# Kernel optimization log

Measured on AMD Instinct MI355X. Metric: run time of the kernel, lower is better.

## Reference

```python
import jax, jax.numpy as jnp
import numpy as np
from jax import lax

EPS = 1e-4
DN = ('NDHWC', 'DHWIO', 'NDHWC')


def _m(mask, dtype):
    return mask[..., None].astype(dtype)


def bn_relu(x, mask):
    # BatchNorm1d over active voxels only (training-mode batch stats, gamma=1, beta=0), then ReLU.
    m = _m(mask, x.dtype)
    n = jnp.sum(m)
    mean = jnp.sum(x * m, axis=(0, 1, 2, 3)) / n
    xc = (x - mean) * m  # re-mask: inactive voxels stay exactly zero
    var = jnp.sum(xc * xc, axis=(0, 1, 2, 3)) / n
    return jnp.maximum(xc * lax.rsqrt(var + EPS), 0.0)


def subm3(x, w, mask):
    # SubMConv3d k=3 pad=1: dense conv on zero-at-inactive input, output restricted to active sites.
    y = lax.conv_general_dilated(x, w, (1, 1, 1), 'SAME', dimension_numbers=DN)
    return y * _m(mask, x.dtype)


def down2(x, w):
    # SparseConv3d k=2 s=2: non-overlapping windows; inactive inputs are zero so dense strided conv matches.
    return lax.conv_general_dilated(x, w, (2, 2, 2), 'VALID', dimension_numbers=DN)


def pool_mask(mask):
    B, D, H, W = mask.shape
    return jnp.any(mask.reshape(B, D // 2, 2, H // 2, 2, W // 2, 2), axis=(2, 4, 6))


def up2(x, w, mask):
    # SparseInverseConv3d k=2 (indice_key inverse of the stride-2 conv): conv-transpose masked to original indices.
    y = jnp.einsum('bdhwc,ijkco->bdihjwko', x, w)
    B, Dc, _, Hc, _, Wc, _, Co = y.shape
    return y.reshape(B, 2 * Dc, 2 * Hc, 2 * Wc, Co) * _m(mask, x.dtype)


def resblock(x, mask, wa, wb, w_sc=None):
    # ResidualBlock: i_branch (identity or 1x1 Custom1x1Subm3d: feats @ W.T) + BN-ReLU-SubM-BN-ReLU-SubM.
    idb = x if w_sc is None else jnp.einsum('bdhwc,oc->bdhwo', x, w_sc)
    h = bn_relu(x, mask)
    h = subm3(h, wa, mask)
    h = bn_relu(h, mask)
    h = subm3(h, wb, mask)
    return h + idb


def unet_forward(x, mask, w_in, w_b1a, w_b1b, w_d1, w_b2a, w_b2b, w_d2,
                 w_b3a, w_b3b, w_u2, w_t2_sc, w_t2a, w_t2b, w_u1, w_t1_sc, w_t1a, w_t1b):
    mask2 = pool_mask(mask)
    mask3 = pool_mask(mask2)
    x0 = subm3(x, w_in, mask)                 # input_conv (subm1)
    x1 = resblock(x0, mask, w_b1a, w_b1b)     # level-1 block (32->32)
    d1 = down2(bn_relu(x1, mask), w_d1)       # BN-ReLU + stride-2 conv 32->64
    x2 = resblock(d1, mask2, w_b2a, w_b2b)    # level-2 block (64->64)
    d2 = down2(bn_relu(x2, mask2), w_d2)      # 64->96
    x3 = resblock(d2, mask3, w_b3a, w_b3b)    # bottom level (96->96)
    u2 = up2(bn_relu(x3, mask3), w_u2, mask2)  # BN-ReLU + inverse conv 96->64
    t2 = resblock(jnp.concatenate([x2, u2], -1), mask2, w_t2a, w_t2b, w_t2_sc)  # tail 128->64
    u1 = up2(bn_relu(t2, mask2), w_u1, mask)   # 64->32
    t1 = resblock(jnp.concatenate([x1, u1], -1), mask, w_t1a, w_t1b, w_t1_sc)   # tail 64->32
    return bn_relu(t1, mask)                   # output_layer: BN + ReLU


def setup_inputs() -> dict:
    key = jax.random.key(0)
    ks = jax.random.split(key, 20)
    B, D = 1, 48
    Cin, C1, C2, C3 = 6, 32, 64, 96
    mask = jax.random.uniform(ks[0], (B, D, D, D)) < 0.12
    x = jax.random.normal(ks[1], (B, D, D, D, Cin), jnp.float32) * mask[..., None]

    def w(k, shape):
        fan = float(np.prod(shape[:-1]))
        return (jax.random.normal(k, shape, jnp.float32) / np.sqrt(fan)).astype(jnp.float32)

    return {
        'x': x, 'mask': mask,
        'w_in': w(ks[2], (3, 3, 3, Cin, C1)),
        'w_b1a': w(ks[3], (3, 3, 3, C1, C1)), 'w_b1b': w(ks[4], (3, 3, 3, C1, C1)),
        'w_d1': w(ks[5], (2, 2, 2, C1, C2)),
        'w_b2a': w(ks[6], (3, 3, 3, C2, C2)), 'w_b2b': w(ks[7], (3, 3, 3, C2, C2)),
        'w_d2': w(ks[8], (2, 2, 2, C2, C3)),
        'w_b3a': w(ks[9], (3, 3, 3, C3, C3)), 'w_b3b': w(ks[10], (3, 3, 3, C3, C3)),
        'w_u2': w(ks[11], (2, 2, 2, C3, C2)),
        'w_t2_sc': w(ks[12], (C2, 2 * C2)),
        'w_t2a': w(ks[13], (3, 3, 3, 2 * C2, C2)), 'w_t2b': w(ks[14], (3, 3, 3, C2, C2)),
        'w_u1': w(ks[15], (2, 2, 2, C2, C1)),
        'w_t1_sc': w(ks[16], (C1, 2 * C1)),
        'w_t1a': w(ks[17], (3, 3, 3, 2 * C1, C1)), 'w_t1b': w(ks[18], (3, 3, 3, C1, C1)),
    }


def reference(x, mask, w_in, w_b1a, w_b1b, w_d1, w_b2a, w_b2b, w_d2,
              w_b3a, w_b3b, w_u2, w_t2_sc, w_t2a, w_t2b, w_u1, w_t1_sc, w_t1a, w_t1b):
    return unet_forward(x, mask, w_in, w_b1a, w_b1b, w_d1, w_b2a, w_b2b, w_d2,
                        w_b3a, w_b3b, w_u2, w_t2_sc, w_t2a, w_t2b, w_u1, w_t1_sc, w_t1a, w_t1b)
```

## Files before the change

### kernel.cpp

```cpp
#include <hip/hip_runtime.h>


typedef short bf16x8 __attribute__((ext_vector_type(8)));
typedef float f32x4 __attribute__((ext_vector_type(4)));
typedef unsigned short ushort_t;

constexpr int D1 = 48, DIM2 = 24, DIM3 = 12;
constexpr int N1 = D1 * D1 * D1;
constexpr int N2 = DIM2 * DIM2 * DIM2;
constexpr int N3 = DIM3 * DIM3 * DIM3;

constexpr size_t OFF_A      = 0;
constexpr size_t OFF_R1     = 3538944;
constexpr size_t OFF_CAT1   = 7077888;
constexpr size_t OFF_D1R    = 14155776;
constexpr size_t OFF_R3     = 15040512;
constexpr size_t OFF_CAT2   = 15925248;
constexpr size_t OFF_D2R    = 17694720;
constexpr size_t OFF_R4     = 17860608;
constexpr size_t OFF_X3R    = 18026496;
constexpr size_t OFF_BN1_32 = 18192384;
constexpr size_t OFF_BN1_64 = 19961920;
constexpr size_t OFF_BN2_A  = 23500928;
constexpr size_t OFF_BN2_B  = 23943360;
constexpr size_t OFF_BN3_96 = 24385792;
constexpr size_t OFF_BFEND  = 24468800;
constexpr size_t OFF_WT     = 24468800;
constexpr size_t OFF_STATS  = 25142592;
constexpr size_t STATS_FLOATS = 16 * 4096;
constexpr size_t OFF_CNT    = OFF_STATS + STATS_FLOATS;
constexpr size_t OFF_L1     = OFF_CNT + 16;
constexpr size_t OFF_L2     = OFF_L1 + N1;
constexpr size_t OFF_L3     = OFF_L2 + N2;
constexpr size_t OFF_M1     = OFF_L3 + N3;
constexpr size_t OFF_M2     = OFF_M1 + N1 / 4;
constexpr size_t OFF_M3     = OFF_M2 + N2 / 4;

constexpr int WTS[17] = {0, 27648, 55296, 82944, 99328, 209920, 320512,
                         369664, 618496, 867328, 977920, 1088512, 1199104,
                         1254400, 1282048, 1331200, 1347584};

__device__ inline ushort_t f2bf(float f) {
  union { float f; unsigned u; } x; x.f = f;
  unsigned u = x.u + 0x7FFF + ((x.u >> 16) & 1);
  return (ushort_t)(u >> 16);
}

__global__ __launch_bounds__(256) void k_mask1(const float* __restrict__ x,
                                               unsigned char* __restrict__ m,
                                               int* __restrict__ list, int* __restrict__ cnt) {
  int v = blockIdx.x * 256 + threadIdx.x;
  if (v >= N1) return;
  const float* p = x + (size_t)v * 6;
  bool a = (p[0] != 0.f) || (p[1] != 0.f) || (p[2] != 0.f) ||
           (p[3] != 0.f) || (p[4] != 0.f) || (p[5] != 0.f);
  m[v] = a ? 1 : 0;
  if (a) { int pos = atomicAdd(cnt, 1); list[pos] = v; }
}

__global__ __launch_bounds__(256) void k_pool(const unsigned char* __restrict__ mf,
                                              unsigned char* __restrict__ mc,
                                              int* __restrict__ list, int* __restrict__ cnt, int DC) {
  int v = blockIdx.x * 256 + threadIdx.x;
  int n = DC * DC * DC;
  if (v >= n) return;
  int w = v % DC, h = (v / DC) % DC, d = v / (DC * DC);
  int DF = 2 * DC;
  bool a = false;
  for (int i = 0; i < 2; i++)
    for (int j = 0; j < 2; j++)
      for (int k = 0; k < 2; k++)
        a |= (mf[(size_t)(((2 * d + i) * DF + (2 * h + j)) * DF + (2 * w + k))] != 0);
  mc[v] = a ? 1 : 0;
  if (a) { int pos = atomicAdd(cnt, 1); list[pos] = v; }
}

struct WJobs {
  const float* src[16];
  int start[17];
  short cirtot[16], cio[16], cipad[16], cout[16];
};

__global__ __launch_bounds__(256) void k_wprep(WJobs jb, ushort_t* __restrict__ wt, int total) {
  int gid = blockIdx.x * 256 + threadIdx.x;
  if (gid >= total) return;
  int j = 0;
#pragma unroll
  for (int jj = 0; jj < 16; jj++)
    if (gid >= jb.start[jj + 1]) j = jj + 1;
  int e = gid - jb.start[j];
  int CIP = jb.cipad[j], CO = jb.cout[j];
  int CIRT = jb.cirtot[j], CIO = jb.cio[j];
  int ci = e % CIP;
  int co = (e / CIP) % CO;
  int k = e / (CIP * CO);
  float v = (ci + CIO < CIRT) ? jb.src[j][((size_t)k * CIRT + CIO + ci) * CO + co] : 0.f;
  wt[gid] = f2bf(v);
}

__global__ __launch_bounds__(256) void k_xprep(const float* __restrict__ x, ushort_t* __restrict__ xp) {
  int gid = blockIdx.x * 256 + threadIdx.x;
  if (gid >= (N1 + 4) * 8) return;
  int v = gid >> 3, c = (gid & 7) * 4;
  uint2 o = make_uint2(0u, 0u);
  if (v < N1) {
    ushort_t u[4];
#pragma unroll
    for (int j = 0; j < 4; j++) {
      int ci = c + j;
      float f = (ci < 6) ? x[(size_t)v * 6 + ci] : 0.f;
      u[j] = f2bf(f);
    }
    o.x = (unsigned)u[0] | ((unsigned)u[1] << 16);
    o.y = (unsigned)u[2] | ((unsigned)u[3] << 16);
  }
  *(uint2*)&xp[(size_t)v * 32 + c] = o;
}

template <int CIPAD, int CB, int KK, int DD, bool UP>
__global__ __launch_bounds__(512, 2) void k_conv7(
    const ushort_t* __restrict__ in, const ushort_t* __restrict__ wt, int cot,
    float* __restrict__ out, int ostride, int ooff,
    const float* __restrict__ res, int rstride,
    double* __restrict__ st,
    const int* __restrict__ list, const int* __restrict__ cnt) {
  constexpr int KCH = CIPAD / 32;
  constexpr int NCO = CB / 16;
  constexpr int TPS = (KK + 3) / 4;
  constexpr int BUNITS = KK * KCH * CB * 4;
  __shared__ ushort_t blds[BUNITS * 8];
  __shared__ float red[4][2][NCO * 4][64];
  __shared__ float sred0[CB], sred1[CB];
  __shared__ int vidx[32];

  int n = cnt[0];
  int t = threadIdx.x, wv = t >> 6, ln = t & 63;
  int vg = wv & 1, ks = wv >> 1;
  int fr = ln & 15, kg = ln >> 4;
  int coblk = blockIdx.y * CB;

  for (int e = t; e < BUNITS; e += 512) {
    int kgs = e & 3;
    int co = (e >> 2) % CB;
    int r2 = (e >> 2) / CB;
    int c = r2 % KCH;
    int k = r2 / KCH;
    bf16x8 w = *(const bf16x8*)(wt + ((size_t)k * cot + coblk + co) * CIPAD + c * 32 + kgs * 8);
    *(bf16x8*)(blds + (size_t)e * 8) = w;
  }
  if (t < CB) { sred0[t] = 0.f; sred1[t] = 0.f; }
  __syncthreads();

  float smr = 0.f, sqr = 0.f;
  int myco = ((t >> 8) % NCO) * 16 + (t & 15);

  for (int tile = blockIdx.x; tile * 32 < n; tile += gridDim.x) {
    int base = tile * 32;
    if (t < 32) vidx[t] = (base + t < n) ? list[base + t] : -1;
    __syncthreads();

    int av = vidx[vg * 16 + fr];
    int vv = av < 0 ? 0 : av;
    int ad = vv / (DD * DD), ah = (vv / DD) % DD, aw = vv % DD;
    int pidx = 0, corner = -1;
    if (UP) {
      constexpr int DC = DD / 2;
      pidx = (((ad >> 1) * DC) + (ah >> 1)) * DC + (aw >> 1);
      corner = ((ad & 1) << 2) | ((ah & 1) << 1) | (aw & 1);
    }
    constexpr int GDI = UP ? (DD / 2) : ((KK == 8) ? 2 * DD : DD);
    constexpr int SENT = GDI * GDI * GDI;

    const int k0 = ks * TPS;
    auto nixOf = [&](int kq) -> int {
      int kc = (kq < KK) ? kq : KK - 1;
      if (UP) {
        return (av >= 0 && corner == kc) ? pidx : SENT;
      } else if (KK == 27) {
        int kd = kc / 9 - 1, kh = (kc / 3) % 3 - 1, kw = kc % 3 - 1;
        int nd = ad + kd, nh = ah + kh, nw = aw + kw;
        bool inb = (av >= 0) && (unsigned)nd < (unsigned)DD &&
                   (unsigned)nh < (unsigned)DD && (unsigned)nw < (unsigned)DD;
        return inb ? (nd * DD + nh) * DD + nw : SENT;
      } else {
        return (av >= 0) ? ((2 * ad + ((kc >> 2) & 1)) * GDI + (2 * ah + ((kc >> 1) & 1))) * GDI +
                               (2 * aw + (kc & 1))
                         : SENT;
      }
    };
    auto loadA = [&](bf16x8* dst, int kq) {
      int nix = nixOf(kq);
      const ushort_t* ap = in + (size_t)nix * CIPAD + kg * 8;
#pragma unroll
      for (int c = 0; c < KCH; c++) dst[c] = *(const bf16x8*)(ap + c * 32);
    };

    f32x4 acc[NCO];
#pragma unroll
    for (int f = 0; f < NCO; f++) acc[f] = (f32x4){0.f, 0.f, 0.f, 0.f};

    bf16x8 aA[KCH], aB[KCH];
    loadA(aA, k0);
#pragma unroll
    for (int j = 0; j < TPS; j++) {
      bf16x8* cur = (j & 1) ? aB : aA;
      bf16x8* nxt = (j & 1) ? aA : aB;
      if (j + 1 < TPS) loadA(nxt, k0 + j + 1);
      if (k0 + j < KK) {
#pragma unroll
        for (int c = 0; c < KCH; c++) {
#pragma unroll
          for (int f = 0; f < NCO; f++) {
            bf16x8 b = *(const bf16x8*)(blds +
                ((((size_t)((k0 + j) * KCH + c) * CB) + f * 16 + fr) * 4 + kg) * 8);
            acc[f] = __builtin_amdgcn_mfma_f32_16x16x32_bf16(cur[c], b, acc[f], 0, 0, 0);
          }
        }
      }
    }

#pragma unroll
    for (int f = 0; f < NCO; f++)
#pragma unroll
      for (int r = 0; r < 4; r++)
        red[ks][vg][f * 4 + r][ln] = acc[f][r];
    __syncthreads();

#pragma unroll
    for (int e0 = 0; e0 < NCO; e0++) {
      int e = t + e0 * 512;
      int ln2 = e & 63, r = (e >> 6) & 3;
      int f = (e >> 8) % NCO;
      int vg2 = e / (256 * NCO);
      int ei = f * 4 + r;
      float s = red[0][vg2][ei][ln2] + red[1][vg2][ei][ln2] +
                red[2][vg2][ei][ln2] + red[3][vg2][ei][ln2];
      int slot = vg2 * 16 + (ln2 >> 4) * 4 + r;
      int co = f * 16 + (ln2 & 15);
      int v = vidx[slot];
      if (v >= 0) {
        int gco = coblk + co;
        float val = s;
        if (res) val += res[(size_t)v * rstride + gco];
        out[(size_t)v * ostride + ooff + gco] = val;
        smr += val; sqr += val * val;
      }
    }
    __syncthreads();
  }

  atomicAdd(&sred0[myco], smr);
  atomicAdd(&sred1[myco], sqr);
  __syncthreads();
  if (t < CB) {
    double* sr = st + (size_t)(blockIdx.x & 7) * 256;
    atomicAdd(&sr[coblk + t], (double)sred0[t]);
    atomicAdd(&sr[128 + coblk + t], (double)sred1[t]);
  }
}

template <int C>
__global__ __launch_bounds__(256) void k_bnapply2(
    const float* __restrict__ x, int xstr, int coff,
    const double* __restrict__ sA, const double* __restrict__ sB, int csplit,
    const int* __restrict__ list, const int* __restrict__ cnt,
    ushort_t* __restrict__ out) {
  __shared__ float mu_s[C], inv_s[C];
  int n = cnt[0];
  int t = threadIdx.x;
  if (t < C) {
    const double* s = (t < csplit) ? (sA + t) : (sB + (t - csplit));
    double sm = 0.0, sq = 0.0;
#pragma unroll
    for (int r = 0; r < 8; r++) { sm += s[r * 256]; sq += s[r * 256 + 128]; }
    double mu = sm / n;
    double var = sq / n - mu * mu;
    mu_s[t] = (float)mu;
    inv_s[t] = rsqrtf((float)fmax(var, 0.0) + 1e-4f);
  }
  __syncthreads();
  int total = n * (C / 4);
  for (int gid = blockIdx.x * 256 + t; gid < total; gid += gridDim.x * 256) {
    int i = gid / (C / 4);
    int c = (gid % (C / 4)) * 4;
    int v = list[i];
    float4 xv = *(const float4*)&x[(size_t)v * xstr + coff + c];
    float xa[4] = {xv.x, xv.y, xv.z, xv.w};
    ushort_t u[4];
#pragma unroll
    for (int j = 0; j < 4; j++)
      u[j] = f2bf(fmaxf((xa[j] - mu_s[c + j]) * inv_s[c + j], 0.f));
    uint2 o; o.x = (unsigned)u[0] | ((unsigned)u[1] << 16);
    o.y = (unsigned)u[2] | ((unsigned)u[3] << 16);
    *(uint2*)&out[(size_t)v * C + c] = o;
  }
}

__global__ __launch_bounds__(256) void k_bnout(const float* __restrict__ x,
                                               const unsigned char* __restrict__ m,
                                               const double* __restrict__ s,
                                               const int* __restrict__ cnt,
                                               float* __restrict__ out) {
  __shared__ float mu_s[32], inv_s[32];
  int t = threadIdx.x;
  int n = cnt[0];
  if (t < 32) {
    double sm = 0.0, sq = 0.0;
#pragma unroll
    for (int r = 0; r < 8; r++) { sm += s[r * 256 + t]; sq += s[r * 256 + 128 + t]; }
    double mu = sm / n;
    double var = sq / n - mu * mu;
    mu_s[t] = (float)mu;
    inv_s[t] = rsqrtf((float)fmax(var, 0.0) + 1e-4f);
  }
  __syncthreads();
  int gid = blockIdx.x * 256 + t;
  if (gid >= N1 * 8) return;
  int v = gid / 8;
  int c = (gid % 8) * 4;
  float4 o = make_float4(0.f, 0.f, 0.f, 0.f);
  if (m[v]) {
    float4 xv = *(const float4*)&x[(size_t)v * 32 + c];
    o.x = fmaxf((xv.x - mu_s[c + 0]) * inv_s[c + 0], 0.f);
    o.y = fmaxf((xv.y - mu_s[c + 1]) * inv_s[c + 1], 0.f);
    o.z = fmaxf((xv.z - mu_s[c + 2]) * inv_s[c + 2], 0.f);
    o.w = fmaxf((xv.w - mu_s[c + 3]) * inv_s[c + 3], 0.f);
  }
  *(float4*)&out[(size_t)v * 32 + c] = o;
}

template <int CI, int CO>
__global__ __launch_bounds__(256) void k_sc(const float* __restrict__ in,
                                            const float* __restrict__ wsc,
                                            float* __restrict__ out,
                                            const int* __restrict__ list,
                                            const int* __restrict__ cnt) {
  int n = cnt[0];
  long total = (long)n * CO;
  for (long gid = (long)blockIdx.x * 256 + threadIdx.x; gid < total; gid += (long)gridDim.x * 256) {
    int i = (int)(gid / CO), o = (int)(gid % CO);
    int v = list[i];
    const float4* xr = (const float4*)(in + (size_t)v * CI);
    const float4* wr = (const float4*)(wsc + (size_t)o * CI);
    float a = 0.f;
    for (int c = 0; c < CI / 4; c++) {
      float4 x4 = xr[c], w4 = wr[c];
      a += x4.x * w4.x + x4.y * w4.y + x4.z * w4.z + x4.w * w4.w;
    }
    out[(size_t)v * CO + o] = a;
  }
}

extern "C" void kernel_launch(void* const* d_in, const int* in_sizes, int n_in,
                              void* d_out, int out_size, void* d_ws, size_t ws_size,
                              hipStream_t stream) {
  float* W = (float*)d_ws;
  const float* x = (const float*)d_in[0];

  float* A    = W + OFF_A;
  float* R1   = W + OFF_R1;
  float* CAT1 = W + OFF_CAT1;
  float* D1R  = W + OFF_D1R;
  float* R3   = W + OFF_R3;
  float* CAT2 = W + OFF_CAT2;
  float* D2R  = W + OFF_D2R;
  float* R4   = W + OFF_R4;
  float* X3R  = W + OFF_X3R;
  ushort_t* XP     = (ushort_t*)(W + OFF_CAT1);
  ushort_t* BN1_32 = (ushort_t*)(W + OFF_BN1_32);
  ushort_t* BN1_64 = (ushort_t*)(W + OFF_BN1_64);
  ushort_t* BN2A   = (ushort_t*)(W + OFF_BN2_A);
  ushort_t* BN2B   = (ushort_t*)(W + OFF_BN2_B);
  ushort_t* BN3_96 = (ushort_t*)(W + OFF_BN3_96);
  ushort_t* WT  = (ushort_t*)(W + OFF_WT);
  double* S0 = (double*)(W + OFF_STATS);
  int* CNT = (int*)(W + OFF_CNT);
  int* L1 = (int*)(W + OFF_L1);
  int* L2 = (int*)(W + OFF_L2);
  int* L3 = (int*)(W + OFF_L3);
  unsigned char* M1 = (unsigned char*)(W + OFF_M1);
  unsigned char* M2 = (unsigned char*)(W + OFF_M2);
  unsigned char* M3 = (unsigned char*)(W + OFF_M3);

  auto S = [&](int i) { return S0 + (size_t)i * 2048; };

  hipMemsetAsync(W + OFF_STATS, 0, (STATS_FLOATS + 16) * 4, stream);
  hipMemsetAsync(W + OFF_BN1_32, 0, (OFF_BFEND - OFF_BN1_32) * 4, stream);

  k_mask1<<<N1 / 256, 256, 0, stream>>>(x, M1, L1, CNT + 0);
  k_pool<<<N2 / 256, 256, 0, stream>>>(M1, M2, L2, CNT + 1, DIM2);
  k_pool<<<(N3 + 255) / 256, 256, 0, stream>>>(M2, M3, L3, CNT + 2, DIM3);

  WJobs jb;
  const int srcIdx[16]  = {2, 3, 4, 5, 6, 7, 8, 9, 10, 13, 13, 14, 17, 18, 11, 15};
  const short cirtot[16]= {6, 32, 32, 32, 64, 64, 64, 96, 96, 128, 128, 64, 64, 32, 96, 64};
  const short cio[16]   = {0, 0, 0, 0, 0, 0, 0, 0, 0, 0, 64, 0, 0, 0, 0, 0};
  const short cipad[16] = {32, 32, 32, 32, 64, 64, 64, 96, 96, 64, 64, 64, 64, 32, 96, 64};
  const short couts[16] = {32, 32, 32, 64, 64, 64, 96, 96, 96, 64, 64, 64, 32, 32, 64, 32};
  for (int j = 0; j < 16; j++) {
    jb.src[j] = (const float*)d_in[srcIdx[j]];
    jb.cirtot[j] = cirtot[j]; jb.cio[j] = cio[j];
    jb.cipad[j] = cipad[j]; jb.cout[j] = couts[j];
    jb.start[j] = WTS[j];
  }
  jb.start[16] = WTS[16];
  k_wprep<<<(WTS[16] + 255) / 256, 256, 0, stream>>>(jb, WT, WTS[16]);
  k_xprep<<<((N1 + 4) * 8 + 255) / 256, 256, 0, stream>>>(x, XP);

  const int BNG = 512;

  k_conv7<32, 32, 27, D1, false><<<dim3(256, 1), 512, 0, stream>>>(
      XP, WT + WTS[0], 32, A, 32, 0, nullptr, 0, S(0), L1, CNT + 0);
  k_bnapply2<32><<<BNG, 256, 0, stream>>>(A, 32, 0, S(0), S(0), 32, L1, CNT + 0, BN1_32);
  k_conv7<32, 32, 27, D1, false><<<dim3(256, 1), 512, 0, stream>>>(
      BN1_32, WT + WTS[1], 32, R1, 32, 0, nullptr, 0, S(1), L1, CNT + 0);
  k_bnapply2<32><<<BNG, 256, 0, stream>>>(R1, 32, 0, S(1), S(1), 32, L1, CNT + 0, BN1_32);
  k_conv7<32, 32, 27, D1, false><<<dim3(256, 1), 512, 0, stream>>>(
      BN1_32, WT + WTS[2], 32, CAT1, 64, 0, A, 32, S(2), L1, CNT + 0);
  k_bnapply2<32><<<BNG, 256, 0, stream>>>(CAT1, 64, 0, S(2), S(2), 32, L1, CNT + 0, BN1_32);
  k_conv7<32, 32, 8, DIM2, false><<<dim3(128, 2), 512, 0, stream>>>(
      BN1_32, WT + WTS[3], 64, D1R, 64, 0, nullptr, 0, S(3), L2, CNT + 1);

  k_bnapply2<64><<<BNG, 256, 0, stream>>>(D1R, 64, 0, S(3), S(3), 64, L2, CNT + 1, BN2A);
  k_conv7<64, 32, 27, DIM2, false><<<dim3(128, 2), 512, 0, stream>>>(
      BN2A, WT + WTS[4], 64, R3, 64, 0, nullptr, 0, S(4), L2, CNT + 1);
  k_bnapply2<64><<<BNG, 256, 0, stream>>>(R3, 64, 0, S(4), S(4), 64, L2, CNT + 1, BN2A);
  k_conv7<64, 32, 27, DIM2, false><<<dim3(128, 2), 512, 0, stream>>>(
      BN2A, WT + WTS[5], 64, CAT2, 128, 0, D1R, 64, S(5), L2, CNT + 1);
  k_bnapply2<64><<<BNG, 256, 0, stream>>>(CAT2, 128, 0, S(5), S(5), 64, L2, CNT + 1, BN2A);
  k_conv7<64, 32, 8, DIM3, false><<<dim3(54, 3), 512, 0, stream>>>(
      BN2A, WT + WTS[6], 96, D2R, 96, 0, nullptr, 0, S(6), L3, CNT + 2);

  k_bnapply2<96><<<BNG, 256, 0, stream>>>(D2R, 96, 0, S(6), S(6), 96, L3, CNT + 2, BN3_96);
  k_conv7<96, 16, 27, DIM3, false><<<dim3(54, 6), 512, 0, stream>>>(
      BN3_96, WT + WTS[7], 96, R4, 96, 0, nullptr, 0, S(7), L3, CNT + 2);
  k_bnapply2<96><<<BNG, 256, 0, stream>>>(R4, 96, 0, S(7), S(7), 96, L3, CNT + 2, BN3_96);
  k_conv7<96, 16, 27, DIM3, false><<<dim3(54, 6), 512, 0, stream>>>(
      BN3_96, WT + WTS[8], 96, X3R, 96, 0, D2R, 96, S(8), L3, CNT + 2);
  k_bnapply2<96><<<BNG, 256, 0, stream>>>(X3R, 96, 0, S(8), S(8), 96, L3, CNT + 2, BN3_96);
  k_conv7<96, 32, 8, DIM2, true><<<dim3(128, 2), 512, 0, stream>>>(
      BN3_96, WT + WTS[14], 64, CAT2, 128, 64, nullptr, 0, S(9), L2, CNT + 1);

  k_bnapply2<64><<<BNG, 256, 0, stream>>>(CAT2, 128, 64, S(9), S(9), 64, L2, CNT + 1, BN2B);
  k_conv7<64, 32, 27, DIM2, false><<<dim3(128, 2), 512, 0, stream>>>(
      BN2A, WT + WTS[9], 64, R3, 64, 0, nullptr, 0, S(15), L2, CNT + 1);
  k_conv7<64, 32, 27, DIM2, false><<<dim3(128, 2), 512, 0, stream>>>(
      BN2B, WT + WTS[10], 64, R3, 64, 0, R3, 64, S(10), L2, CNT + 1);
  k_bnapply2<64><<<BNG, 256, 0, stream>>>(R3, 64, 0, S(10), S(10), 64, L2, CNT + 1, BN2A);
  k_sc<128, 64><<<512, 256, 0, stream>>>(CAT2, (const float*)d_in[12], D1R, L2, CNT + 1);
  k_conv7<64, 32, 27, DIM2, false><<<dim3(128, 2), 512, 0, stream>>>(
      BN2A, WT + WTS[11], 64, R3, 64, 0, D1R, 64, S(11), L2, CNT + 1);
  k_bnapply2<64><<<BNG, 256, 0, stream>>>(R3, 64, 0, S(11), S(11), 64, L2, CNT + 1, BN2A);
  k_conv7<64, 32, 8, D1, true><<<dim3(256, 1), 512, 0, stream>>>(
      BN2A, WT + WTS[15], 32, CAT1, 64, 32, nullptr, 0, S(12), L1, CNT + 0);

  k_bnapply2<64><<<BNG, 256, 0, stream>>>(CAT1, 64, 0, S(2), S(12), 32, L1, CNT + 0, BN1_64);
  k_conv7<64, 32, 27, D1, false><<<dim3(256, 1), 512, 0, stream>>>(
      BN1_64, WT + WTS[12], 32, R1, 32, 0, nullptr, 0, S(13), L1, CNT + 0);
  k_bnapply2<32><<<BNG, 256, 0, stream>>>(R1, 32, 0, S(13), S(13), 32, L1, CNT + 0, BN1_32);
  k_sc<64, 32><<<512, 256, 0, stream>>>(CAT1, (const float*)d_in[16], A, L1, CNT + 0);
  k_conv7<32, 32, 27, D1, false><<<dim3(256, 1), 512, 0, stream>>>(
      BN1_32, WT + WTS[13], 32, A, 32, 0, A, 32, S(14), L1, CNT + 0);
  k_bnout<<<N1 * 8 / 256, 256, 0, stream>>>(A, M1, S(14), CNT + 0, (float*)d_out);
}
```

Baseline: 391.6 us.

## Hold conv weights in registers instead of LDS and parameterize voxel-group split

The sparse conv kernel now loads each wave's slice of the weights straight into registers (indexed by its tap range) instead of staging all taps in shared memory and reading B fragments from LDS inside the MFMA loop. A new VG template parameter controls how the 8 waves divide between voxel groups and tap splits. Channel-block sizes and grid shapes for several layers are retuned to match. This removes the LDS weight staging, its barrier and the per-MFMA LDS reads, but raises register pressure (up to TPS*KCH*NCO bf16x8 per lane), which could cause spills or lower occupancy under launch_bounds(512,2).

```diff
diff --git a/kernel.cpp b/kernel.cpp
--- a/kernel.cpp
+++ b/kernel.cpp
@@ -117,8 +117,8 @@
   *(uint2*)&xp[(size_t)v * 32 + c] = o;
 }
 
-template <int CIPAD, int CB, int KK, int DD, bool UP>
-__global__ __launch_bounds__(512, 2) void k_conv7(
+template <int CIPAD, int CB, int KK, int VG, int DD, bool UP>
+__global__ __launch_bounds__(512, 2) void k_conv8(
     const ushort_t* __restrict__ in, const ushort_t* __restrict__ wt, int cot,
     float* __restrict__ out, int ostride, int ooff,
     const float* __restrict__ res, int rstride,
@@ -126,37 +126,45 @@
     const int* __restrict__ list, const int* __restrict__ cnt) {
   constexpr int KCH = CIPAD / 32;
   constexpr int NCO = CB / 16;
-  constexpr int TPS = (KK + 3) / 4;
-  constexpr int BUNITS = KK * KCH * CB * 4;
-  __shared__ ushort_t blds[BUNITS * 8];
-  __shared__ float red[4][2][NCO * 4][64];
+  constexpr int KS = 8 / VG;
+  constexpr int TPS = (KK + KS - 1) / KS;
+  constexpr int TILE = VG * 16;
+  constexpr int ETOT = VG * NCO * 256;
+  constexpr int NE = (ETOT + 511) / 512;
+  __shared__ float red[KS][VG][NCO * 4][64];
   __shared__ float sred0[CB], sred1[CB];
-  __shared__ int vidx[32];
+  __shared__ int vidx[TILE];
 
   int n = cnt[0];
   int t = threadIdx.x, wv = t >> 6, ln = t & 63;
-  int vg = wv & 1, ks = wv >> 1;
+  int vg = wv % VG, ks = wv / VG;
   int fr = ln & 15, kg = ln >> 4;
   int coblk = blockIdx.y * CB;
-
-  for (int e = t; e < BUNITS; e += 512) {
-    int kgs = e & 3;
-    int co = (e >> 2) % CB;
-    int r2 = (e >> 2) / CB;
-    int c = r2 % KCH;
-    int k = r2 / KCH;
-    bf16x8 w = *(const bf16x8*)(wt + ((size_t)k * cot + coblk + co) * CIPAD + c * 32 + kgs * 8);
-    *(bf16x8*)(blds + (size_t)e * 8) = w;
+  int k0 = ks * TPS;
+
+  bf16x8 wr[TPS][KCH][NCO];
+#pragma unroll
+  for (int j = 0; j < TPS; j++) {
+    int kk = k0 + j;
+    int kc = (kk < KK) ? kk : KK - 1;
+#pragma unroll
+    for (int c = 0; c < KCH; c++)
+#pragma unroll
+      for (int f = 0; f < NCO; f++)
+        wr[j][c][f] = *(const bf16x8*)(wt +
+            ((size_t)kc * cot + coblk + f * 16 + fr) * CIPAD + c * 32 + kg * 8);
   }
   if (t < CB) { sred0[t] = 0.f; sred1[t] = 0.f; }
-  __syncthreads();
 
   float smr = 0.f, sqr = 0.f;
   int myco = ((t >> 8) % NCO) * 16 + (t & 15);
 
-  for (int tile = blockIdx.x; tile * 32 < n; tile += gridDim.x) {
-    int base = tile * 32;
-    if (t < 32) vidx[t] = (base + t < n) ? list[base + t] : -1;
+  constexpr int GDI = UP ? (DD / 2) : ((KK == 8) ? 2 * DD : DD);
+  constexpr int SENT = GDI * GDI * GDI;
+
+  for (int tile = blockIdx.x; tile * TILE < n; tile += gridDim.x) {
+    int base = tile * TILE;
+    if (t < TILE) vidx[t] = (base + t < n) ? list[base + t] : -1;
     __syncthreads();
 
     int av = vidx[vg * 16 + fr];
@@ -168,28 +176,26 @@
       pidx = (((ad >> 1) * DC) + (ah >> 1)) * DC + (aw >> 1);
       corner = ((ad & 1) << 2) | ((ah & 1) << 1) | (aw & 1);
     }
-    constexpr int GDI = UP ? (DD / 2) : ((KK == 8) ? 2 * DD : DD);
-    constexpr int SENT = GDI * GDI * GDI;
-
-    const int k0 = ks * TPS;
+
     auto nixOf = [&](int kq) -> int {
       int kc = (kq < KK) ? kq : KK - 1;
+      bool tapv = (kq < KK) && (av >= 0);
       if (UP) {
-        return (av >= 0 && corner == kc) ? pidx : SENT;
+        return (tapv && corner == kc) ? pidx : SENT;
       } else if (KK == 27) {
         int kd = kc / 9 - 1, kh = (kc / 3) % 3 - 1, kw = kc % 3 - 1;
         int nd = ad + kd, nh = ah + kh, nw = aw + kw;
-        bool inb = (av >= 0) && (unsigned)nd < (unsigned)DD &&
+        bool inb = tapv && (unsigned)nd < (unsigned)DD &&
                    (unsigned)nh < (unsigned)DD && (unsigned)nw < (unsigned)DD;
         return inb ? (nd * DD + nh) * DD + nw : SENT;
       } else {
-        return (av >= 0) ? ((2 * ad + ((kc >> 2) & 1)) * GDI + (2 * ah + ((kc >> 1) & 1))) * GDI +
-                               (2 * aw + (kc & 1))
-                         : SENT;
+        return tapv ? ((2 * ad + ((kc >> 2) & 1)) * GDI + (2 * ah + ((kc >> 1) & 1))) * GDI +
+                          (2 * aw + (kc & 1))
+                    : SENT;
       }
     };
-    auto loadA = [&](bf16x8* dst, int kq) {
-      int nix = nixOf(kq);
+    auto loadA = [&](bf16x8* dst, int j) {
+      int nix = nixOf(k0 + j);
       const ushort_t* ap = in + (size_t)nix * CIPAD + kg * 8;
 #pragma unroll
       for (int c = 0; c < KCH; c++) dst[c] = *(const bf16x8*)(ap + c * 32);
@@ -200,23 +206,16 @@
     for (int f = 0; f < NCO; f++) acc[f] = (f32x4){0.f, 0.f, 0.f, 0.f};
 
     bf16x8 aA[KCH], aB[KCH];
-    loadA(aA, k0);
+    loadA(aA, 0);
 #pragma unroll
     for (int j = 0; j < TPS; j++) {
+      if (j + 1 < TPS) loadA((j & 1) ? aA : aB, j + 1);
       bf16x8* cur = (j & 1) ? aB : aA;
-      bf16x8* nxt = (j & 1) ? aA : aB;
-      if (j + 1 < TPS) loadA(nxt, k0 + j + 1);
-      if (k0 + j < KK) {
-#pragma unroll
-        for (int c = 0; c < KCH; c++) {
-#pragma unroll
-          for (int f = 0; f < NCO; f++) {
-            bf16x8 b = *(const bf16x8*)(blds +
-                ((((size_t)((k0 + j) * KCH + c) * CB) + f * 16 + fr) * 4 + kg) * 8);
-            acc[f] = __builtin_amdgcn_mfma_f32_16x16x32_bf16(cur[c], b, acc[f], 0, 0, 0);
-          }
-        }
-      }
+#pragma unroll
+      for (int c = 0; c < KCH; c++)
+#pragma unroll
+        for (int f = 0; f < NCO; f++)
+          acc[f] = __builtin_amdgcn_mfma_f32_16x16x32_bf16(cur[c], wr[j][c][f], acc[f], 0, 0, 0);
     }
 
 #pragma unroll
@@ -227,23 +226,25 @@
     __syncthreads();
 
 #pragma unroll
-    for (int e0 = 0; e0 < NCO; e0++) {
+    for (int e0 = 0; e0 < NE; e0++) {
       int e = t + e0 * 512;
-      int ln2 = e & 63, r = (e >> 6) & 3;
-      int f = (e >> 8) % NCO;
-      int vg2 = e / (256 * NCO);
-      int ei = f * 4 + r;
-      float s = red[0][vg2][ei][ln2] + red[1][vg2][ei][ln2] +
-                red[2][vg2][ei][ln2] + red[3][vg2][ei][ln2];
-      int slot = vg2 * 16 + (ln2 >> 4) * 4 + r;
-      int co = f * 16 + (ln2 & 15);
-      int v = vidx[slot];
-      if (v >= 0) {
-        int gco = coblk + co;
-        float val = s;
-        if (res) val += res[(size_t)v * rstride + gco];
-        out[(size_t)v * ostride + ooff + gco] = val;
-        smr += val; sqr += val * val;
+      if (e < ETOT) {
+        int ln2 = e & 63, r = (e >> 6) & 3;
+        int f = (e >> 8) % NCO;
+        int vg2 = e / (256 * NCO);
+        float s = 0.f;
+#pragma unroll
+        for (int q = 0; q < KS; q++) s += red[q][vg2][f * 4 + r][ln2];
+        int slot = vg2 * 16 + (ln2 >> 4) * 4 + r;
+        int co = f * 16 + (ln2 & 15);
+        int v = vidx[slot];
+        if (v >= 0) {
+          int gco = coblk + co;
+          float val = s;
+          if (res) val += res[(size_t)v * rstride + gco];
+          out[(size_t)v * ostride + ooff + gco] = val;
+          smr += val; sqr += val * val;
+        }
       }
     }
     __syncthreads();
@@ -409,57 +410,57 @@
 
   const int BNG = 512;
 
-  k_conv7<32, 32, 27, D1, false><<<dim3(256, 1), 512, 0, stream>>>(
+  k_conv8<32, 32, 27, 2, D1, false><<<dim3(256, 1), 512, 0, stream>>>(
       XP, WT + WTS[0], 32, A, 32, 0, nullptr, 0, S(0), L1, CNT + 0);
   k_bnapply2<32><<<BNG, 256, 0, stream>>>(A, 32, 0, S(0), S(0), 32, L1, CNT + 0, BN1_32);
-  k_conv7<32, 32, 27, D1, false><<<dim3(256, 1), 512, 0, stream>>>(
+  k_conv8<32, 32, 27, 2, D1, false><<<dim3(256, 1), 512, 0, stream>>>(
       BN1_32, WT + WTS[1], 32, R1, 32, 0, nullptr, 0, S(1), L1, CNT + 0);
   k_bnapply2<32><<<BNG, 256, 0, stream>>>(R1, 32, 0, S(1), S(1), 32, L1, CNT + 0, BN1_32);
-  k_conv7<32, 32, 27, D1, false><<<dim3(256, 1), 512, 0, stream>>>(
+  k_conv8<32, 32, 27, 2, D1, false><<<dim3(256, 1), 512, 0, stream>>>(
       BN1_32, WT + WTS[2], 32, CAT1, 64, 0, A, 32, S(2), L1, CNT + 0);
   k_bnapply2<32><<<BNG, 256, 0, stream>>>(CAT1, 64, 0, S(2), S(2), 32, L1, CNT + 0, BN1_32);
-  k_conv7<32, 32, 8, DIM2, false><<<dim3(128, 2), 512, 0, stream>>>(
+  k_conv8<32, 32, 8, 2, DIM2, false><<<dim3(160, 2), 512, 0, stream>>>(
       BN1_32, WT + WTS[3], 64, D1R, 64, 0, nullptr, 0, S(3), L2, CNT + 1);
 
   k_bnapply2<64><<<BNG, 256, 0, stream>>>(D1R, 64, 0, S(3), S(3), 64, L2, CNT + 1, BN2A);
-  k_conv7<64, 32, 27, DIM2, false><<<dim3(128, 2), 512, 0, stream>>>(
+  k_conv8<64, 16, 27, 2, DIM2, false><<<dim3(96, 4), 512, 0, stream>>>(
       BN2A, WT + WTS[4], 64, R3, 64, 0, nullptr, 0, S(4), L2, CNT + 1);
   k_bnapply2<64><<<BNG, 256, 0, stream>>>(R3, 64, 0, S(4), S(4), 64, L2, CNT + 1, BN2A);
-  k_conv7<64, 32, 27, DIM2, false><<<dim3(128, 2), 512, 0, stream>>>(
+  k_conv8<64, 16, 27, 2, DIM2, false><<<dim3(96, 4), 512, 0, stream>>>(
       BN2A, WT + WTS[5], 64, CAT2, 128, 0, D1R, 64, S(5), L2, CNT + 1);
   k_bnapply2<64><<<BNG, 256, 0, stream>>>(CAT2, 128, 0, S(5), S(5), 64, L2, CNT + 1, BN2A);
-  k_conv7<64, 32, 8, DIM3, false><<<dim3(54, 3), 512, 0, stream>>>(
+  k_conv8<64, 32, 8, 2, DIM3, false><<<dim3(54, 3), 512, 0, stream>>>(
       BN2A, WT + WTS[6], 96, D2R, 96, 0, nullptr, 0, S(6), L3, CNT + 2);
 
   k_bnapply2<96><<<BNG, 256, 0, stream>>>(D2R, 96, 0, S(6), S(6), 96, L3, CNT + 2, BN3_96);
-  k_conv7<96, 16, 27, DIM3, false><<<dim3(54, 6), 512, 0, stream>>>(
+  k_conv8<96, 16, 27, 1, DIM3, false><<<dim3(108, 6), 512, 0, stream>>>(
       BN3_96, WT + WTS[7], 96, R4, 96, 0, nullptr, 0, S(7), L3, CNT + 2);
   k_bnapply2<96><<<BNG, 256, 0, stream>>>(R4, 96, 0, S(7), S(7), 96, L3, CNT + 2, BN3_96);
-  k_conv7<96, 16, 27, DIM3, false><<<dim3(54, 6), 512, 0, stream>>>(
+  k_conv8<96, 16, 27, 1, DIM3, false><<<dim3(108, 6), 512, 0, stream>>>(
       BN3_96, WT + WTS[8], 96, X3R, 96, 0, D2R, 96, S(8), L3, CNT + 2);
   k_bnapply2<96><<<BNG, 256, 0, stream>>>(X3R, 96, 0, S(8), S(8), 96, L3, CNT + 2, BN3_96);
-  k_conv7<96, 32, 8, DIM2, true><<<dim3(128, 2), 512, 0, stream>>>(
+  k_conv8<96, 32, 8, 2, DIM2, true><<<dim3(160, 2), 512, 0, stream>>>(
       BN3_96, WT + WTS[14], 64, CAT2, 128, 64, nullptr, 0, S(9), L2, CNT + 1);
 
   k_bnapply2<64><<<BNG, 256, 0, stream>>>(CAT2, 128, 64, S(9), S(9), 64, L2, CNT + 1, BN2B);
-  k_conv7<64, 32, 27, DIM2, false><<<dim3(128, 2), 512, 0, stream>>>(
+  k_conv8<64, 16, 27, 2, DIM2, false><<<dim3(96, 4), 512, 0, stream>>>(
       BN2A, WT + WTS[9], 64, R3, 64, 0, nullptr, 0, S(15), L2, CNT + 1);
-  k_conv7<64, 32, 27, DIM2, false><<<dim3(128, 2), 512, 0, stream>>>(
+  k_conv8<64, 16, 27, 2, DIM2, false><<<dim3(96, 4), 512, 0, stream>>>(
       BN2B, WT + WTS[10], 64, R3, 64, 0, R3, 64, S(10), L2, CNT + 1);
   k_bnapply2<64><<<BNG, 256, 0, stream>>>(R3, 64, 0, S(10), S(10), 64, L2, CNT + 1, BN2A);
   k_sc<128, 64><<<512, 256, 0, stream>>>(CAT2, (const float*)d_in[12], D1R, L2, CNT + 1);
-  k_conv7<64, 32, 27, DIM2, false><<<dim3(128, 2), 512, 0, stream>>>(
+  k_conv8<64, 16, 27, 2, DIM2, false><<<dim3(96, 4), 512, 0, stream>>>(
       BN2A, WT + WTS[11], 64, R3, 64, 0, D1R, 64, S(11), L2, CNT + 1);
   k_bnapply2<64><<<BNG, 256, 0, stream>>>(R3, 64, 0, S(11), S(11), 64, L2, CNT + 1, BN2A);
-  k_conv7<64, 32, 8, D1, true><<<dim3(256, 1), 512, 0, stream>>>(
+  k_conv8<64, 32, 8, 2, D1, true><<<dim3(256, 1), 512, 0, stream>>>(
       BN2A, WT + WTS[15], 32, CAT1, 64, 32, nullptr, 0, S(12), L1, CNT + 0);
 
   k_bnapply2<64><<<BNG, 256, 0, stream>>>(CAT1, 64, 0, S(2), S(12), 32, L1, CNT + 0, BN1_64);
-  k_conv7<64, 32, 27, D1, false><<<dim3(256, 1), 512, 0, stream>>>(
+  k_conv8<64, 16, 27, 2, D1, false><<<dim3(256, 2), 512, 0, stream>>>(
       BN1_64, WT + WTS[12], 32, R1, 32, 0, nullptr, 0, S(13), L1, CNT + 0);
   k_bnapply2<32><<<BNG, 256, 0, stream>>>(R1, 32, 0, S(13), S(13), 32, L1, CNT + 0, BN1_32);
   k_sc<64, 32><<<512, 256, 0, stream>>>(CAT1, (const float*)d_in[16], A, L1, CNT + 0);
-  k_conv7<32, 32, 27, D1, false><<<dim3(256, 1), 512, 0, stream>>>(
+  k_conv8<32, 32, 27, 2, D1, false><<<dim3(256, 1), 512, 0, stream>>>(
       BN1_32, WT + WTS[13], 32, A, 32, 0, A, 32, S(14), L1, CNT + 0);
   k_bnout<<<N1 * 8 / 256, 256, 0, stream>>>(A, M1, S(14), CNT + 0, (float*)d_out);
 }
```

Measured after the change: 423.6 us. +8.2%, slower.
